# Performance work log

Hardware: AMD Instinct MI355X
Metric: run time of the kernel (lower is better)

Reference implementation:

```python
import jax, jax.numpy as jnp
import numpy as np

N = 8192       # number of nodes (dense NxN attention)
F_IN = 256     # input feature dim
F_OUT = 64     # projected feature dim (F_prime)
NEG_SLOPE = 0.01  # nn.LeakyReLU default


def setup_inputs() -> dict:
    key = jax.random.key(0)
    k0, k1, k2, k3 = jax.random.split(key, 4)
    H = jax.random.normal(k0, (N, F_IN), dtype=jnp.float32)
    # dense 0/1 adjacency; force self-loops so every row has a nonzero denominator
    A = jax.random.randint(k1, (N, N), 0, 2, dtype=jnp.int32)
    A = jnp.maximum(A, jnp.eye(N, dtype=jnp.int32))
    # learned params: W : F_IN -> F_OUT (self.W), a : 2*F_OUT -> 1 (self.a)
    W = jax.random.normal(k2, (F_IN, F_OUT), dtype=jnp.float32) / np.sqrt(F_IN)
    bW = jnp.zeros((F_OUT,), dtype=jnp.float32)
    a_w = jax.random.normal(k3, (2 * F_OUT,), dtype=jnp.float32) / np.sqrt(2 * F_OUT)
    a_b = jnp.zeros((), dtype=jnp.float32)
    return {"H": H, "A": A, "W": W, "bW": bW, "a_w": a_w, "a_b": a_b}


def reference(H, A, W, bW, a_w, a_b):
    # Wh[i] = W(H[i])  -> [N, F_OUT]
    Wh = H @ W + bW
    # a([Wh_i ; Wh_j]) = a1.Wh_i + a2.Wh_j + a_b : decompose the concat-linear
    s_src = Wh @ a_w[:F_OUT]           # [N]
    s_tar = Wh @ a_w[F_OUT:]           # [N]
    logits = s_src[:, None] + s_tar[None, :] + a_b   # [N, N]
    # e_ij = exp(leaky_relu(logits))
    e = jnp.exp(jnp.where(logits >= 0, logits, NEG_SLOPE * logits))
    # denominator masks by adjacency (sum_j e_ij * A_ij), as in the original
    denom = jnp.sum(e * A.astype(e.dtype), axis=1, keepdims=True)  # [N, 1]
    alpha = e / denom                   # NOTE: numerator NOT masked (faithful)
    # H'_i = sigmoid(alpha_i @ Wh)
    return jax.nn.sigmoid(alpha @ Wh)   # [N, F_OUT]
```

## Files before the change

### kernel.cpp

```cpp
#include <hip/hip_runtime.h>

#define NN 8192
#define FIN 256
#define FOUT 64
#define NRANK 256
#define NBLK 1024
#define NUNITS 1024

typedef int iv4 __attribute__((ext_vector_type(4)));

__global__ __launch_bounds__(256) void k1_proj(
    const float* __restrict__ H, const float* __restrict__ W,
    const float* __restrict__ bW, const float* __restrict__ aw,
    const float* __restrict__ ab,
    float* __restrict__ Wh, float* __restrict__ s_src, float* __restrict__ t_tar,
    float* __restrict__ E1, float* __restrict__ E2, float* __restrict__ PP,
    unsigned* __restrict__ ctrs)
{
    __shared__ float Hs[16 * FIN];
    int tid = threadIdx.x;
    if (blockIdx.x == 0 && tid < 4) ctrs[tid] = 0u;
    int i0 = blockIdx.x * 16;
    const float4* Hv = (const float4*)(H + (size_t)i0 * FIN);
    float4* Hsv = (float4*)Hs;
    for (int idx = tid; idx < 16 * FIN / 4; idx += 256) Hsv[idx] = Hv[idx];
    __syncthreads();
    int f = tid & 63, sub = tid >> 6;
    float a1f = aw[f], a2f = aw[64 + f];
    float b = bW[f];
    float acc0 = b, acc1 = b, acc2 = b, acc3 = b;
    for (int k = 0; k < FIN; ++k) {
        float w = W[k * FOUT + f];
        acc0 += Hs[(sub     ) * FIN + k] * w;
        acc1 += Hs[(sub +  4) * FIN + k] * w;
        acc2 += Hs[(sub +  8) * FIN + k] * w;
        acc3 += Hs[(sub + 12) * FIN + k] * w;
    }
    float accs[4] = {acc0, acc1, acc2, acc3};
    #pragma unroll
    for (int q = 0; q < 4; ++q) {
        int i = i0 + sub + 4 * q;
        float a = accs[q];
        Wh[(size_t)i * FOUT + f] = a;
        float v1 = a * a1f, v2 = a * a2f;
        #pragma unroll
        for (int o = 32; o > 0; o >>= 1) {
            v1 += __shfl_xor(v1, o);
            v2 += __shfl_xor(v2, o);
        }
        if (f == 0) {
            float s = v1 + ab[0];
            float t = v2;
            s_src[i] = s; t_tar[i] = t;
            E1[i] = __expf(s); E2[i] = __expf(0.01f * s);
            PP[2 * i]     = __expf(t);
            PP[2 * i + 1] = __expf(0.01f * t);
        }
    }
}

__global__ __launch_bounds__(256, 4) void kA_rank_denom(
    const int* __restrict__ A,
    const float* __restrict__ t_tar, const float* __restrict__ s_src,
    const float* __restrict__ PP,
    const float* __restrict__ E1, const float* __restrict__ E2,
    int* __restrict__ sorted_idx, int* __restrict__ kidx,
    float* __restrict__ denom, unsigned* __restrict__ ctrs)
{
    __shared__ float Ts[NN];
    __shared__ float red[4][8][2];
    __shared__ unsigned ucur;
    int tid = threadIdx.x, wv = tid >> 6, lane = tid & 63;
    int b = blockIdx.x;

    if (b < NRANK) {
        const float4* tv = (const float4*)t_tar;
        float4* Tsv = (float4*)Ts;
        for (int idx = tid; idx < NN / 4; idx += 256) Tsv[idx] = tv[idx];
        __syncthreads();
        int g0 = b * 32 + wv * 8;
        float tj[8], thr[8];
        int rk[8], kc[8];
        #pragma unroll
        for (int q = 0; q < 8; ++q) {
            tj[q] = Ts[g0 + q];
            thr[q] = -s_src[g0 + q];
            rk[q] = 0; kc[q] = 0;
        }
        for (int k = lane; k < NN; k += 64) {
            float tk = Ts[k];
            #pragma unroll
            for (int q = 0; q < 8; ++q) {
                rk[q] += (tk < tj[q] || (tk == tj[q] && k < g0 + q)) ? 1 : 0;
                kc[q] += (tk < thr[q]) ? 1 : 0;
            }
        }
        #pragma unroll
        for (int q = 0; q < 8; ++q) {
            #pragma unroll
            for (int o = 32; o > 0; o >>= 1) {
                rk[q] += __shfl_xor(rk[q], o);
                kc[q] += __shfl_xor(kc[q], o);
            }
        }
        if (lane == 0) {
            #pragma unroll
            for (int q = 0; q < 8; ++q) {
                sorted_idx[rk[q]] = g0 + q;
                kidx[g0 + q] = kc[q];
            }
        }
    }

    for (;;) {
        if (tid == 0) ucur = atomicAdd(&ctrs[0], 1u);
        __syncthreads();
        unsigned u = ucur;
        __syncthreads();
        if (u >= NUNITS) break;
        int i0 = (int)u * 8;
        float e1r[8], accA[8], accB[8];
        #pragma unroll
        for (int r = 0; r < 8; ++r) { e1r[r] = E1[i0 + r]; accA[r] = 0.f; accB[r] = 0.f; }
        const float4* PPv = (const float4*)PP;
        for (int jv = tid; jv < NN / 4; jv += 256) {
            float4 ppA = PPv[2 * jv];
            float4 ppB = PPv[2 * jv + 1];
            #pragma unroll
            for (int r = 0; r < 8; ++r) {
                const iv4 a4 = __builtin_nontemporal_load(
                    (const iv4*)(A + (size_t)(i0 + r) * NN + jv * 4));
                float e1 = e1r[r];
                {
                    bool c = e1 * ppA.x >= 1.0f;
                    float af = (float)a4.x;
                    accA[r] += af * (c ? ppA.x : 0.0f);
                    accB[r] += af * (c ? 0.0f : ppA.y);
                }
                {
                    bool c = e1 * ppA.z >= 1.0f;
                    float af = (float)a4.y;
                    accA[r] += af * (c ? ppA.z : 0.0f);
                    accB[r] += af * (c ? 0.0f : ppA.w);
                }
                {
                    bool c = e1 * ppB.x >= 1.0f;
                    float af = (float)a4.z;
                    accA[r] += af * (c ? ppB.x : 0.0f);
                    accB[r] += af * (c ? 0.0f : ppB.y);
                }
                {
                    bool c = e1 * ppB.z >= 1.0f;
                    float af = (float)a4.w;
                    accA[r] += af * (c ? ppB.z : 0.0f);
                    accB[r] += af * (c ? 0.0f : ppB.w);
                }
            }
        }
        #pragma unroll
        for (int r = 0; r < 8; ++r) {
            #pragma unroll
            for (int o = 32; o > 0; o >>= 1) {
                accA[r] += __shfl_xor(accA[r], o);
                accB[r] += __shfl_xor(accB[r], o);
            }
        }
        if ((tid & 63) == 0) {
            #pragma unroll
            for (int r = 0; r < 8; ++r) { red[wv][r][0] = accA[r]; red[wv][r][1] = accB[r]; }
        }
        __syncthreads();
        if (tid < 8) {
            float sA = red[0][tid][0] + red[1][tid][0] + red[2][tid][0] + red[3][tid][0];
            float sB = red[0][tid][1] + red[1][tid][1] + red[2][tid][1] + red[3][tid][1];
            denom[i0 + tid] = E1[i0 + tid] * sA + E2[i0 + tid] * sB;
        }
        __syncthreads();
    }
}

__global__ __launch_bounds__(64) void k3a_tots(
    const float* __restrict__ Wh, const float* __restrict__ PP,
    const int* __restrict__ sorted_idx,
    float* __restrict__ tots1, float* __restrict__ tots2)
{
    int c = blockIdx.x, f = threadIdx.x;
    float t1 = 0.f, t2 = 0.f;
    int m0 = c * 32;
    #pragma unroll 8
    for (int m = m0; m < m0 + 32; ++m) {
        int sj = sorted_idx[m];
        float wh = Wh[(size_t)sj * 64 + f];
        t1 += PP[2 * sj]     * wh;
        t2 += PP[2 * sj + 1] * wh;
    }
    tots1[c * 64 + f] = t1; tots2[c * 64 + f] = t2;
}

__global__ __launch_bounds__(64) void k3bc_emit(
    const float* __restrict__ Wh, const float* __restrict__ PP,
    const int* __restrict__ sorted_idx,
    const float* __restrict__ tots1, const float* __restrict__ tots2,
    float* __restrict__ pre2, float* __restrict__ suf1)
{
    int c = blockIdx.x, f = threadIdx.x;
    float o2 = 0.f;
    #pragma unroll 8
    for (int w = 0; w < c; ++w) o2 += tots2[w * 64 + f];
    float o1 = 0.f;
    #pragma unroll 8
    for (int w = c + 1; w < 256; ++w) o1 += tots1[w * 64 + f];
    int m0 = c * 32;
    float whr[32], p1r[32], p2r[32];
    #pragma unroll
    for (int q = 0; q < 32; ++q) {
        int sj = sorted_idx[m0 + q];
        whr[q] = Wh[(size_t)sj * 64 + f];
        p1r[q] = PP[2 * sj]; p2r[q] = PP[2 * sj + 1];
    }
    float run2 = o2;
    #pragma unroll
    for (int q = 0; q < 32; ++q) {
        pre2[(size_t)(m0 + q) * 64 + f] = run2;
        run2 += p2r[q] * whr[q];
    }
    if (c == 255) pre2[(size_t)NN * 64 + f] = run2;
    float run1 = o1;
    #pragma unroll
    for (int q = 31; q >= 0; --q) {
        run1 += p1r[q] * whr[q];
        suf1[(size_t)(m0 + q) * 64 + f] = run1;
    }
    if (c == 255) suf1[(size_t)NN * 64 + f] = 0.f;
}

__global__ __launch_bounds__(256) void k5_out(
    const float* __restrict__ suf1, const float* __restrict__ pre2,
    const int* __restrict__ kidx, const float* __restrict__ E1,
    const float* __restrict__ E2, const float* __restrict__ denom,
    float* __restrict__ out)
{
    int tid = threadIdx.x;
    int f = tid & 63, sub = tid >> 6;
    int i = blockIdx.x * 4 + sub;
    int k = kidx[i];
    float num = E1[i] * suf1[(size_t)k * 64 + f] + E2[i] * pre2[(size_t)k * 64 + f];
    float x = num / denom[i];
    out[(size_t)i * 64 + f] = 1.0f / (1.0f + __expf(-x));
}

extern "C" void kernel_launch(void* const* d_in, const int* in_sizes, int n_in,
                              void* d_out, int out_size, void* d_ws, size_t ws_size,
                              hipStream_t stream) {
    const float* H  = (const float*)d_in[0];
    const int*   A  = (const int*)d_in[1];
    const float* W  = (const float*)d_in[2];
    const float* bW = (const float*)d_in[3];
    const float* aw = (const float*)d_in[4];
    const float* ab = (const float*)d_in[5];
    float* out = (float*)d_out;

    float* ws    = (float*)d_ws;
    float* Wh    = ws;
    float* s_src = Wh + 524288;
    float* t_tar = s_src + 8192;
    float* E1    = t_tar + 8192;
    float* E2    = E1 + 8192;
    float* PP    = E2 + 8192;
    float* pre2  = PP + 16384;
    float* suf1  = pre2 + 524352;
    float* tots1 = suf1 + 524352;
    float* tots2 = tots1 + 16384;
    float* denom = tots2 + 16384;
    int* sorted_idx = (int*)(denom + 8192);
    int* kidx       = sorted_idx + 8192;
    unsigned* ctrs  = (unsigned*)(kidx + 8192);

    hipLaunchKernelGGL(k1_proj, dim3(512), dim3(256), 0, stream,
                       H, W, bW, aw, ab, Wh, s_src, t_tar, E1, E2, PP, ctrs);
    hipLaunchKernelGGL(kA_rank_denom, dim3(NBLK), dim3(256), 0, stream,
                       A, t_tar, s_src, PP, E1, E2, sorted_idx, kidx, denom, ctrs);
    hipLaunchKernelGGL(k3a_tots, dim3(256), dim3(64), 0, stream,
                       Wh, PP, sorted_idx, tots1, tots2);
    hipLaunchKernelGGL(k3bc_emit, dim3(256), dim3(64), 0, stream,
                       Wh, PP, sorted_idx, tots1, tots2, pre2, suf1);
    hipLaunchKernelGGL(k5_out, dim3(2048), dim3(256), 0, stream,
                       suf1, pre2, kidx, E1, E2, denom, out);
}
```

Measured before the change: 409.3 us.

## Fuse prefix/suffix scan kernels into rank kernel with grid barriers

Folds the per-chunk totals and prefix/suffix emit stages into the rank blocks of the main kernel. Two software grid barriers on atomic counters synchronise the 256 rank blocks, and the denominator work queue moves to a separate counter. This removes two kernel launches and their round trips through global memory. It also vectorises the projection inner loop with float4 shared-memory reads. The trade-off is that the denominator work is delayed on the blocks that wait at the barriers, and the kernel can deadlock if all 256 rank blocks are not resident at once.

Result: slower. 452.1 us (+10.5%).

```diff
diff --git a/kernel.cpp b/kernel.cpp
--- a/kernel.cpp
+++ b/kernel.cpp
@@ -29,12 +29,21 @@
     float a1f = aw[f], a2f = aw[64 + f];
     float b = bW[f];
     float acc0 = b, acc1 = b, acc2 = b, acc3 = b;
-    for (int k = 0; k < FIN; ++k) {
-        float w = W[k * FOUT + f];
-        acc0 += Hs[(sub     ) * FIN + k] * w;
-        acc1 += Hs[(sub +  4) * FIN + k] * w;
-        acc2 += Hs[(sub +  8) * FIN + k] * w;
-        acc3 += Hs[(sub + 12) * FIN + k] * w;
+    const float4* h0v = (const float4*)(Hs + (sub     ) * FIN);
+    const float4* h1v = (const float4*)(Hs + (sub +  4) * FIN);
+    const float4* h2v = (const float4*)(Hs + (sub +  8) * FIN);
+    const float4* h3v = (const float4*)(Hs + (sub + 12) * FIN);
+    #pragma unroll 4
+    for (int k4 = 0; k4 < FIN / 4; ++k4) {
+        float4 h0 = h0v[k4], h1 = h1v[k4], h2 = h2v[k4], h3 = h3v[k4];
+        float w0 = W[(4 * k4 + 0) * FOUT + f];
+        float w1 = W[(4 * k4 + 1) * FOUT + f];
+        float w2 = W[(4 * k4 + 2) * FOUT + f];
+        float w3 = W[(4 * k4 + 3) * FOUT + f];
+        acc0 += h0.x * w0 + h0.y * w1 + h0.z * w2 + h0.w * w3;
+        acc1 += h1.x * w0 + h1.y * w1 + h1.z * w2 + h1.w * w3;
+        acc2 += h2.x * w0 + h2.y * w1 + h2.z * w2 + h2.w * w3;
+        acc3 += h3.x * w0 + h3.y * w1 + h3.z * w2 + h3.w * w3;
     }
     float accs[4] = {acc0, acc1, acc2, acc3};
     #pragma unroll
@@ -59,15 +68,18 @@
     }
 }
 
-__global__ __launch_bounds__(256, 4) void kA_rank_denom(
+__global__ __launch_bounds__(256, 4) void kA_fused(
     const int* __restrict__ A,
     const float* __restrict__ t_tar, const float* __restrict__ s_src,
-    const float* __restrict__ PP,
+    const float* __restrict__ Wh, const float* __restrict__ PP,
     const float* __restrict__ E1, const float* __restrict__ E2,
     int* __restrict__ sorted_idx, int* __restrict__ kidx,
+    float* __restrict__ tots1, float* __restrict__ tots2,
+    float* __restrict__ pre2, float* __restrict__ suf1,
     float* __restrict__ denom, unsigned* __restrict__ ctrs)
 {
     __shared__ float Ts[NN];
+    __shared__ float o1p[4][64], o2p[4][64];
     __shared__ float red[4][8][2];
     __shared__ unsigned ucur;
     int tid = threadIdx.x, wv = tid >> 6, lane = tid & 63;
@@ -110,10 +122,80 @@
                 kidx[g0 + q] = kc[q];
             }
         }
+        __syncthreads();
+        if (tid == 0) {
+            __threadfence();
+            atomicAdd(&ctrs[0], 1u);
+            while (__hip_atomic_load(&ctrs[0], __ATOMIC_ACQUIRE, __HIP_MEMORY_SCOPE_AGENT) < NRANK)
+                __builtin_amdgcn_s_sleep(2);
+            __threadfence();
+        }
+        __syncthreads();
+
+        float* whs = Ts;
+        float* p1s = Ts + 2048;
+        float* p2s = Ts + 4096;
+        int m0 = b * 32;
+        float t1p = 0.f, t2p = 0.f;
+        #pragma unroll
+        for (int q = 0; q < 8; ++q) {
+            int m = wv * 8 + q;
+            int sj = sorted_idx[m0 + m];
+            float wh = Wh[(size_t)sj * 64 + lane];
+            float p1 = PP[2 * sj], p2 = PP[2 * sj + 1];
+            whs[m * 64 + lane] = wh;
+            p1s[m * 64 + lane] = p1;
+            p2s[m * 64 + lane] = p2;
+            t1p += p1 * wh; t2p += p2 * wh;
+        }
+        o1p[wv][lane] = t1p; o2p[wv][lane] = t2p;
+        __syncthreads();
+        if (wv == 0) {
+            float t1 = o1p[0][lane] + o1p[1][lane] + o1p[2][lane] + o1p[3][lane];
+            float t2 = o2p[0][lane] + o2p[1][lane] + o2p[2][lane] + o2p[3][lane];
+            tots1[b * 64 + lane] = t1;
+            tots2[b * 64 + lane] = t2;
+        }
+        __syncthreads();
+        if (tid == 0) {
+            __threadfence();
+            atomicAdd(&ctrs[1], 1u);
+            while (__hip_atomic_load(&ctrs[1], __ATOMIC_ACQUIRE, __HIP_MEMORY_SCOPE_AGENT) < NRANK)
+                __builtin_amdgcn_s_sleep(2);
+            __threadfence();
+        }
+        __syncthreads();
+
+        float s1 = 0.f, s2 = 0.f;
+        for (int c = wv * 64; c < wv * 64 + 64; ++c) {
+            if (c < b) s2 += tots2[c * 64 + lane];
+            if (c > b) s1 += tots1[c * 64 + lane];
+        }
+        o1p[wv][lane] = s1; o2p[wv][lane] = s2;
+        __syncthreads();
+        if (wv == 0) {
+            float o1 = o1p[0][lane] + o1p[1][lane] + o1p[2][lane] + o1p[3][lane];
+            float o2 = o2p[0][lane] + o2p[1][lane] + o2p[2][lane] + o2p[3][lane];
+            float run2 = o2;
+            #pragma unroll 8
+            for (int q = 0; q < 32; ++q) {
+                pre2[(size_t)(m0 + q) * 64 + lane] = run2;
+                run2 += p2s[q * 64 + lane] * whs[q * 64 + lane];
+            }
+            if (b == NRANK - 1) pre2[(size_t)NN * 64 + lane] = run2;
+            float run1 = o1;
+            #pragma unroll 8
+            for (int q = 31; q >= 0; --q) {
+                run1 += p1s[q * 64 + lane] * whs[q * 64 + lane];
+                suf1[(size_t)(m0 + q) * 64 + lane] = run1;
+            }
+            if (b == NRANK - 1) suf1[(size_t)NN * 64 + lane] = 0.f;
+        }
+        __syncthreads();
     }
 
     for (;;) {
-        if (tid == 0) ucur = atomicAdd(&ctrs[0], 1u);
+        if (tid == 0) ucur = atomicAdd(&ctrs[2], 1u);
         __syncthreads();
         unsigned u = ucur;
         __syncthreads();
@@ -179,61 +261,6 @@
     }
 }
 
-__global__ __launch_bounds__(64) void k3a_tots(
-    const float* __restrict__ Wh, const float* __restrict__ PP,
-    const int* __restrict__ sorted_idx,
-    float* __restrict__ tots1, float* __restrict__ tots2)
-{
-    int c = blockIdx.x, f = threadIdx.x;
-    float t1 = 0.f, t2 = 0.f;
-    int m0 = c * 32;
-    #pragma unroll 8
-    for (int m = m0; m < m0 + 32; ++m) {
-        int sj = sorted_idx[m];
-        float wh = Wh[(size_t)sj * 64 + f];
-        t1 += PP[2 * sj]     * wh;
-        t2 += PP[2 * sj + 1] * wh;
-    }
-    tots1[c * 64 + f] = t1; tots2[c * 64 + f] = t2;
-}
-
-__global__ __launch_bounds__(64) void k3bc_emit(
-    const float* __restrict__ Wh, const float* __restrict__ PP,
-    const int* __restrict__ sorted_idx,
-    const float* __restrict__ tots1, const float* __restrict__ tots2,
-    float* __restrict__ pre2, float* __restrict__ suf1)
-{
-    int c = blockIdx.x, f = threadIdx.x;
-    float o2 = 0.f;
-    #pragma unroll 8
-    for (int w = 0; w < c; ++w) o2 += tots2[w * 64 + f];
-    float o1 = 0.f;
-    #pragma unroll 8
-    for (int w = c + 1; w < 256; ++w) o1 += tots1[w * 64 + f];
-    int m0 = c * 32;
-    float whr[32], p1r[32], p2r[32];
-    #pragma unroll
-    for (int q = 0; q < 32; ++q) {
-        int sj = sorted_idx[m0 + q];
-        whr[q] = Wh[(size_t)sj * 64 + f];
-        p1r[q] = PP[2 * sj]; p2r[q] = PP[2 * sj + 1];
-    }
-    float run2 = o2;
-    #pragma unroll
-    for (int q = 0; q < 32; ++q) {
-        pre2[(size_t)(m0 + q) * 64 + f] = run2;
-        run2 += p2r[q] * whr[q];
-    }
-    if (c == 255) pre2[(size_t)NN * 64 + f] = run2;
-    float run1 = o1;
-    #pragma unroll
-    for (int q = 31; q >= 0; --q) {
-        run1 += p1r[q] * whr[q];
-        suf1[(size_t)(m0 + q) * 64 + f] = run1;
-    }
-    if (c == 255) suf1[(size_t)NN * 64 + f] = 0.f;
-}
-
 __global__ __launch_bounds__(256) void k5_out(
     const float* __restrict__ suf1, const float* __restrict__ pre2,
     const int* __restrict__ kidx, const float* __restrict__ E1,
@@ -278,12 +305,9 @@
 
     hipLaunchKernelGGL(k1_proj, dim3(512), dim3(256), 0, stream,
                        H, W, bW, aw, ab, Wh, s_src, t_tar, E1, E2, PP, ctrs);
-    hipLaunchKernelGGL(kA_rank_denom, dim3(NBLK), dim3(256), 0, stream,
-                       A, t_tar, s_src, PP, E1, E2, sorted_idx, kidx, denom, ctrs);
-    hipLaunchKernelGGL(k3a_tots, dim3(256), dim3(64), 0, stream,
-                       Wh, PP, sorted_idx, tots1, tots2);
-    hipLaunchKernelGGL(k3bc_emit, dim3(256), dim3(64), 0, stream,
-                       Wh, PP, sorted_idx, tots1, tots2, pre2, suf1);
+    hipLaunchKernelGGL(kA_fused, dim3(NBLK), dim3(256), 0, stream,
+                       A, t_tar, s_src, Wh, PP, E1, E2,
+                       sorted_idx, kidx, tots1, tots2, pre2, suf1, denom, ctrs);
     hipLaunchKernelGGL(k5_out, dim3(2048), dim3(256), 0, stream,
                        suf1, pre2, kidx, E1, E2, denom, out);
 }
```
